# Kernel optimization log

Hardware: AMD Instinct MI355X
Metric: run time of the kernel (lower is better)

## Reference

```python
import jax, jax.numpy as jnp
import numpy as np

HIDDEN = 512
STATE_DIM = 256
H = 8
D = STATE_DIM // H  # 32
B = 8
T = 4096


def setup_inputs() -> dict:
    key = jax.random.key(0)
    ks = jax.random.split(key, 12)
    s = 0.02
    return {
        "hidden_states": jax.random.normal(ks[0], (B, T, HIDDEN), jnp.float32),
        "state": jnp.zeros((B, H, D, D), jnp.float32),
        "W_k": jax.random.normal(ks[1], (STATE_DIM, HIDDEN), jnp.float32) * s,
        "W_v": jax.random.normal(ks[2], (STATE_DIM, HIDDEN), jnp.float32) * s,
        "W_q": jax.random.normal(ks[3], (STATE_DIM, HIDDEN), jnp.float32) * s,
        "W_beta": jax.random.normal(ks[4], (STATE_DIM, HIDDEN), jnp.float32) * s,
        "b_beta": jnp.zeros((STATE_DIM,), jnp.float32),
        "W_alpha": jax.random.normal(ks[5], (STATE_DIM, HIDDEN), jnp.float32) * s,
        "b_alpha": jnp.full((STATE_DIM,), 2.0, jnp.float32),
        "W_out": jax.random.normal(ks[6], (HIDDEN, STATE_DIM), jnp.float32) * s,
        "gate_W": jax.random.normal(ks[7], (STATE_DIM, HIDDEN), jnp.float32) * s,
        "norm_w": jnp.ones((STATE_DIM,), jnp.float32),
    }


def _rms_norm(x, w, eps=1e-6):
    dtype = x.dtype
    xf = x.astype(jnp.float32)
    n = xf * jax.lax.rsqrt(jnp.mean(xf * xf, axis=-1, keepdims=True) + eps)
    return (n * w).astype(dtype)


def reference(hidden_states, state, W_k, W_v, W_q, W_beta, b_beta, W_alpha, b_alpha, W_out, gate_W, norm_w):
    bsz, seq_len, _ = hidden_states.shape
    # projections -> (B, T, H, D)
    k = (hidden_states @ W_k.T).reshape(bsz, seq_len, H, D)
    v = (hidden_states @ W_v.T).reshape(bsz, seq_len, H, D)
    q = (hidden_states @ W_q.T).reshape(bsz, seq_len, H, D)
    beta = jax.nn.sigmoid(hidden_states @ W_beta.T + b_beta).reshape(bsz, seq_len, H, D)
    alpha = jax.nn.sigmoid(hidden_states @ W_alpha.T + b_alpha).reshape(bsz, seq_len, H, D)
    # F.normalize(k, dim=-1) with eps=1e-12
    k = k / jnp.maximum(jnp.linalg.norm(k, axis=-1, keepdims=True), 1e-12)
    gate = hidden_states @ gate_W.T  # (B, T, STATE_DIM)

    # time-major for scan: (T, B, H, D)
    def tm(x):
        return jnp.swapaxes(x, 0, 1)

    def step(S, inp):
        k_t, v_t, q_t, b_t, a_t = inp
        S = S * a_t[..., None]                              # row-wise decay
        pred = jnp.einsum('bhij,bhj->bhi', S, k_t)
        S = S + jnp.einsum('bhi,bhj->bhij', b_t * (v_t - pred), k_t)
        readout = jnp.einsum('bhij,bhj->bhi', S, q_t)       # (B, H, D)
        return S, readout

    S_final, readouts = jax.lax.scan(step, state, (tm(k), tm(v), tm(q), tm(beta), tm(alpha)))
    context = jnp.swapaxes(readouts, 0, 1).reshape(bsz, seq_len, STATE_DIM)
    context = _rms_norm(context, norm_w) * jax.nn.silu(gate)
    output = context @ W_out.T
    return output, S_final
```

## Files before the change

kernel.cpp:

```cpp
#include <hip/hip_runtime.h>
#include <stdint.h>

#define B_    8
#define T_    4096
#define HID   512
#define SD    256
#define NH    8
#define HD    32
#define M_TOK (B_*T_)

typedef __attribute__((ext_vector_type(8))) short short8;
typedef __attribute__((ext_vector_type(4))) float f32x4;
typedef __attribute__((ext_vector_type(4))) float f4;
typedef __attribute__((ext_vector_type(2))) float f2;

__device__ __forceinline__ unsigned short f2bf(float f) {
  uint32_t u = __float_as_uint(f);
  uint32_t r = (u + 0x7fffu + ((u >> 16) & 1u)) >> 16;
  return (unsigned short)r;
}

__device__ __forceinline__ void gload16(const void* g, void* l) {
  __builtin_amdgcn_global_load_lds((const __attribute__((address_space(1))) void*)g,
                                   (__attribute__((address_space(3))) void*)l,
                                   16, 0, 0);
}

__device__ __forceinline__ float qred16(float x) {
  x += __int_as_float(__builtin_amdgcn_mov_dpp(__float_as_int(x), 0xB1,  0xF, 0xF, true));
  x += __int_as_float(__builtin_amdgcn_mov_dpp(__float_as_int(x), 0x4E,  0xF, 0xF, true));
  x += __int_as_float(__builtin_amdgcn_mov_dpp(__float_as_int(x), 0x141, 0xF, 0xF, true));
  x += __int_as_float(__builtin_amdgcn_mov_dpp(__float_as_int(x), 0x128, 0xF, 0xF, true));
  return x;
}

__device__ __forceinline__ float dpp_xor1(float x) {
  return __int_as_float(__builtin_amdgcn_mov_dpp(__float_as_int(x), 0xB1, 0xF, 0xF, true));
}

__global__ void cvt_f32_bf16(const float* __restrict__ in, unsigned short* __restrict__ out, int n4) {
  int i = blockIdx.x * blockDim.x + threadIdx.x;
  int stride = gridDim.x * blockDim.x;
  for (; i < n4; i += stride) {
    float4 v = reinterpret_cast<const float4*>(in)[i];
    ushort4 o;
    o.x = f2bf(v.x); o.y = f2bf(v.y); o.z = f2bf(v.z); o.w = f2bf(v.w);
    reinterpret_cast<ushort4*>(out)[i] = o;
  }
}

__global__ void __launch_bounds__(256) cvt_weights(
    const float* __restrict__ W_k, const float* __restrict__ W_v,
    const float* __restrict__ W_q, const float* __restrict__ W_beta,
    const float* __restrict__ W_alpha, const float* __restrict__ gate_W,
    const float* __restrict__ W_out,
    unsigned short* __restrict__ Wc, unsigned short* __restrict__ Wob)
{
  int slice = blockIdx.y;
  const float* src = (slice == 0) ? W_k : (slice == 1) ? W_v : (slice == 2) ? W_q :
                     (slice == 3) ? W_beta : (slice == 4) ? W_alpha : (slice == 5) ? gate_W : W_out;
  unsigned short* dst = (slice == 6) ? Wob : (Wc + slice * 131072);
  int i = blockIdx.x * 256 + threadIdx.x;
  float4 v = reinterpret_cast<const float4*>(src)[i];
  ushort4 o;
  o.x = f2bf(v.x); o.y = f2bf(v.y); o.z = f2bf(v.z); o.w = f2bf(v.w);
  reinterpret_cast<ushort4*>(dst)[i] = o;
}

#define PM 128
#define PN 64
#define PK 64

__global__ void __launch_bounds__(256) proj_gemm(
    const unsigned short* __restrict__ hb, const unsigned short* __restrict__ Wc,
    const float* __restrict__ b_beta, const float* __restrict__ b_alpha,
    float* __restrict__ KQi, float* __restrict__ AVBf, float* __restrict__ gate)
{
  __shared__ unsigned short Asm[PM*PK];
  __shared__ unsigned short Bsm[3][PN*PK];
  const int t = threadIdx.x;
  const int w = t >> 6, lane = t & 63;
  const int bm0 = blockIdx.x * PM;
  const int role = blockIdx.y;
  const int grp = role >> 2;
  const int bn0 = (role & 3) * 64;
  const int pr0 = grp ? 4 : 0, pr1 = grp ? 1 : 2, pr2 = grp ? 3 : 5;

  f32x4 acc[3][2][4];
  #pragma unroll
  for (int pp = 0; pp < 3; ++pp)
    #pragma unroll
    for (int i = 0; i < 2; ++i)
      #pragma unroll
      for (int j = 0; j < 4; ++j) acc[pp][i][j] = (f32x4){0.f, 0.f, 0.f, 0.f};

  for (int k0 = 0; k0 < HID; k0 += PK) {
    #pragma unroll
    for (int it = 0; it < 4; ++it) {
      int unit = t + it * 256;
      int row = unit >> 3, seg = unit & 7;
      int dseg = seg ^ (row & 7);
      const unsigned short* g = hb + (size_t)(bm0 + row) * HID + k0 + dseg * 8;
      gload16(g, (char*)Asm + (w * 1024 + it * 4096));
    }
    #pragma unroll
    for (int pp = 0; pp < 3; ++pp) {
      const int pr = (pp == 0) ? pr0 : (pp == 1) ? pr1 : pr2;
      #pragma unroll
      for (int it = 0; it < 2; ++it) {
        int unit = t + it * 256;
        int n = unit >> 3, seg = unit & 7;
        int dseg = seg ^ (n & 7);
        const unsigned short* g = Wc + (size_t)(pr * 256 + bn0 + n) * HID + k0 + dseg * 8;
        gload16(g, (char*)Bsm[pp] + (w * 1024 + it * 4096));
      }
    }
    __syncthreads();
    #pragma unroll
    for (int ks = 0; ks < 2; ++ks) {
      short8 af[2];
      int u = ks * 4 + (lane >> 4);
      int slot = u ^ (lane & 7);
      #pragma unroll
      for (int rb = 0; rb < 2; ++rb) {
        int row = w * 32 + rb * 16 + (lane & 15);
        af[rb] = *(const short8*)((const char*)Asm + row * 128 + slot * 16);
      }
      #pragma unroll
      for (int pp = 0; pp < 3; ++pp) {
        short8 bfr[4];
        #pragma unroll
        for (int cb = 0; cb < 4; ++cb) {
          int nn = cb * 16 + (lane & 15);
          bfr[cb] = *(const short8*)((const char*)Bsm[pp] + nn * 128 + slot * 16);
        }
        #pragma unroll
        for (int rb = 0; rb < 2; ++rb)
          #pragma unroll
          for (int cb = 0; cb < 4; ++cb)
            acc[pp][rb][cb] = __builtin_amdgcn_mfma_f32_16x16x32_bf16(af[rb], bfr[cb], acc[pp][rb][cb], 0, 0, 0);
      }
    }
    __syncthreads();
  }

  if (grp == 0) {
    #pragma unroll
    for (int rb = 0; rb < 2; ++rb) {
      #pragma unroll
      for (int r = 0; r < 4; ++r) {
        float s0 = acc[0][rb][0][r] * acc[0][rb][0][r] + acc[0][rb][1][r] * acc[0][rb][1][r];
        float s1 = acc[0][rb][2][r] * acc[0][rb][2][r] + acc[0][rb][3][r] * acc[0][rb][3][r];
        s0 = qred16(s0); s1 = qred16(s1);
        float i0 = 1.0f / fmaxf(sqrtf(s0), 1e-12f);
        float i1 = 1.0f / fmaxf(sqrtf(s1), 1e-12f);
        acc[0][rb][0][r] *= i0; acc[0][rb][1][r] *= i0;
        acc[0][rb][2][r] *= i1; acc[0][rb][3][r] *= i1;
      }
    }
    #pragma unroll
    for (int rb = 0; rb < 2; ++rb) {
      #pragma unroll
      for (int cb = 0; cb < 4; ++cb) {
        int rem = bn0 + cb * 16 + (lane & 15);
        int h = rem >> 5, d = rem & 31;
        #pragma unroll
        for (int r = 0; r < 4; ++r) {
          int m = bm0 + w * 32 + rb * 16 + (lane >> 4) * 4 + r;
          int bb = m >> 12, tt = m & 4095;
          size_t tok = ((size_t)(bb * NH + h) * T_ + tt);
          float kv = acc[0][rb][cb][r], qv = acc[1][rb][cb][r];
          float kn = dpp_xor1(kv), qn = dpp_xor1(qv);
          if ((lane & 1) == 0)
            *(float4*)&KQi[tok * 64 + (d >> 1) * 4] = (float4){kv, kn, qv, qn};
          gate[(size_t)m * SD + rem] = acc[2][rb][cb][r];
        }
      }
    }
  } else {
    #pragma unroll
    for (int rb = 0; rb < 2; ++rb) {
      #pragma unroll
      for (int cb = 0; cb < 4; ++cb) {
        int rem = bn0 + cb * 16 + (lane & 15);
        int h = rem >> 5, d = rem & 31;
        #pragma unroll
        for (int r = 0; r < 4; ++r) {
          int m = bm0 + w * 32 + rb * 16 + (lane >> 4) * 4 + r;
          int bb = m >> 12, tt = m & 4095;
          size_t tok = ((size_t)(bb * NH + h) * T_ + tt);
          float av = 1.0f / (1.0f + expf(-(acc[0][rb][cb][r] + b_alpha[rem])));
          float vv = acc[1][rb][cb][r];
          float bv = 1.0f / (1.0f + expf(-(acc[2][rb][cb][r] + b_beta[rem])));
          *(float4*)&AVBf[(tok * HD + d) * 4] = (float4){av, vv, bv, 0.0f};
        }
      }
    }
  }
}

#define CH 32
#define NCH (T_/CH)

#define DSR(dst, areg, imm) \
  asm volatile("ds_read_b128 %0, %1 offset:%c2" : "=v"(dst) : "v"(areg), "i"(imm))

#define SHUF2(V,A,B) __builtin_shufflevector(V, V, A, B)

#define BAR asm volatile("s_barrier" ::: "memory")

__global__ void __launch_bounds__(128, 1) scan_kernel(
    const float* __restrict__ KQi, const float4* __restrict__ AVB,
    const float* __restrict__ state_in,
    float* __restrict__ ctx, float* __restrict__ Sfin)
{
  __shared__ __align__(16) char Lds[36864];
  const int blk = blockIdx.x;
  const int bh = blk & 63, rg = blk >> 6;
  const int b = bh >> 3, h = bh & 7;
  const int tid = threadIdx.x;
  const int wid = tid >> 6;
  const int lw = tid & 63;

  const float*  KQg = KQi + (size_t)bh * (T_ * 64);
  const float4* Vg  = AVB + (size_t)bh * (T_ * HD) + rg * 4;

  const uint32_t lds0 = (uint32_t)(uintptr_t)(__attribute__((address_space(3))) char*)&Lds[0];

  if (wid == 1) {
    const int il1 = lw >> 4, tq = lw & 15;
    const uint32_t a_pr = lds0 + 20480 + tq * 256 + il1 * 64;
    float* ctxb = ctx + (size_t)b * T_ * SD + h * HD + rg * 4 + il1;

    const int gpp = lw >> 2, gqt = lw & 3;
    f4 gx0, gx1, gx2, gx3, gy0, gy1, gy2, gy3;
    const uint32_t a_gw = lds0 + 16384 + (2 * gpp) * 64 + gqt * 16 + 12;

    auto stageW = [&](int c2, int buf) {
      const float* kqg = KQg + (size_t)c2 * (CH * 64);
      #pragma unroll
      for (int it = 0; it < 8; ++it)
        gload16(kqg + (size_t)(lw + it * 64) * 4, Lds + buf * 8192 + it * 1024);
      const float4* vg = Vg + (size_t)c2 * (CH * HD);
      #pragma unroll
      for (int it = 0; it < 2; ++it) {
        int tc = it * 16 + (lw >> 2), r = lw & 3;
        gload16(vg + (size_t)tc * HD + r, Lds + 16384 + buf * 2048 + it * 1024);
      }
    };

    auto gfetch = [&](int c2) {
      const float* gp = KQg + ((size_t)c2 * CH + 2 * gpp) * 64 + gqt * 16;
      gx0 = *(const f4*)(gp);      gx1 = *(const f4*)(gp + 4);
      gx2 = *(const f4*)(gp + 8);  gx3 = *(const f4*)(gp + 12);
      gy0 = *(const f4*)(gp + 64); gy1 = *(const f4*)(gp + 68);
      gy2 = *(const f4*)(gp + 72); gy3 = *(const f4*)(gp + 76);
    };

    auto gwrite = [&](int buf) {
      f2 g2 = SHUF2(gx0, 0, 1) * SHUF2(gy0, 0, 1);
      g2 = __builtin_elementwise_fma(SHUF2(gx1, 0, 1), SHUF2(gy1, 0, 1), g2);
      g2 = __builtin_elementwise_fma(SHUF2(gx2, 0, 1), SHUF2(gy2, 0, 1), g2);
      g2 = __builtin_elementwise_fma(SHUF2(gx3, 0, 1), SHUF2(gy3, 0, 1), g2);
      float G = g2.x + g2.y;
      G += __int_as_float(__builtin_amdgcn_mov_dpp(__float_as_int(G), 0xB1, 0xF, 0xF, true));
      G += __int_as_float(__builtin_amdgcn_mov_dpp(__float_as_int(G), 0x4E, 0xF, 0xF, true));
      uint32_t aw = a_gw + buf * 2048;
      asm volatile("ds_write_b32 %0, %1" :: "v"(aw), "v"(G));
      asm volatile("s_waitcnt lgkmcnt(0)" ::: "memory");
    };

#define REDUCE(PB, T0) do { \
      f4 r0_, r1_, r2_, r3_; \
      DSR(r0_, a_pr, (PB)*4096 + 0);  DSR(r1_, a_pr, (PB)*4096 + 16); \
      DSR(r2_, a_pr, (PB)*4096 + 32); DSR(r3_, a_pr, (PB)*4096 + 48); \
      asm volatile("s_waitcnt lgkmcnt(0)" : "+v"(r0_), "+v"(r1_), "+v"(r2_), "+v"(r3_)); \
      f4 s_ = (r0_ + r1_) + (r2_ + r3_); \
      float v_ = (s_.x + s_.y) + (s_.z + s_.w); \
      ctxb[(size_t)((T0) + tq) * SD] = v_; \
    } while (0)

    gfetch(0);
    stageW(0, 0);
    asm volatile("s_waitcnt vmcnt(0)" ::: "memory");
    gwrite(0);
    BAR;
    #pragma unroll 1
    for (int cp = 0; cp < NCH / 2; ++cp) {
      if (cp > 0) REDUCE(2, 64 * cp - 32);
      gfetch(2 * cp + 1);
      stageW(2 * cp + 1, 1);
      BAR;
      if (cp > 0) REDUCE(3, 64 * cp - 16);
      asm volatile("s_waitcnt vmcnt(0)" ::: "memory");
      gwrite(1);
      BAR;
      REDUCE(0, 64 * cp);
      if (cp < NCH / 2 - 1) { gfetch(2 * cp + 2); stageW(2 * cp + 2, 0); }
      BAR;
      REDUCE(1, 64 * cp + 16);
      asm volatile("s_waitcnt vmcnt(0)" ::: "memory");
      if (cp < NCH / 2 - 1) gwrite(0);
      BAR;
    }
    BAR;
    REDUCE(2, T_ - 32);
    REDUCE(3, T_ - 16);
#undef REDUCE
    return;
  }

  const int il = lw >> 4;
  const int p  = lw & 15;

  f2 S2;
  {
    const float* sp = state_in + (size_t)bh * 1024 + (rg * 4 + il) * 32 + p * 2;
    S2 = (f2){sp[0], sp[1]};
  }

  const uint32_t a_kq = lds0 + p * 16;
  const uint32_t a_v  = lds0 + 16384 + il * 16;
  const uint32_t a_pw = lds0 + 20480 + lw * 4;

  f4 kqA, vvA, kqB, vvB, kqC, vvC, kqD, vvD;

#define R2(X, Y, BUF, J) do { \
    DSR(kq##X, a_kq, (BUF)*8192 + (2*(J))*256); \
    DSR(vv##X, a_v,  (BUF)*2048 + (2*(J))*64); \
    DSR(kq##Y, a_kq, (BUF)*8192 + (2*(J)+1)*256); \
    DSR(vv##Y, a_v,  (BUF)*2048 + (2*(J)+1)*64); \
  } while (0)

#define WKA2(N, X, Y) \
    asm volatile("s_waitcnt lgkmcnt(" #N ")" \
                 : "+v"(kq##X), "+v"(vv##X), "+v"(kq##Y), "+v"(vv##Y))

#define C2(X, Y, T0, PB) do { \
    f2 k0_ = SHUF2(kq##X, 0, 1), q0_ = SHUF2(kq##X, 2, 3); \
    f2 k1_ = SHUF2(kq##Y, 0, 1), q1_ = SHUF2(kq##Y, 2, 3); \
    f4 VA_ = vv##X, VB_ = vv##Y; \
    f2 dA_ = k0_ * S2, dB_ = k1_ * S2; \
    float W0_ = qred16(dA_.x + dA_.y); \
    float W1_ = qred16(dB_.x + dB_.y); \
    float u0_ = fmaf(-(VA_.z * VA_.x), W0_, VA_.z * VA_.y); \
    float bua_ = VB_.z * VB_.x; \
    float c2_ = bua_ * VA_.w; \
    float c1_ = fmaf(-(bua_ * VA_.x), W1_, VB_.z * VB_.y); \
    float u1_ = fmaf(-c2_, u0_, c1_); \
    f2 St_ = __builtin_elementwise_fma((f2){u0_, u0_}, k0_, (f2){VA_.x, VA_.x} * S2); \
    f2 Su_ = __builtin_elementwise_fma((f2){u1_, u1_}, k1_, (f2){VB_.x, VB_.x} * St_); \
    f2 o0_ = q0_ * St_; \
    f2 o1_ = q1_ * Su_; \
    float p0_ = o0_.x + o0_.y; \
    float p1_ = o1_.x + o1_.y; \
    S2 = Su_; \
    asm volatile("ds_write_b32 %0, %1 offset:%c2" :: "v"(a_pw), "v"(p0_), "i"((PB)*4096 + ((T0)&15)*256)); \
    asm volatile("ds_write_b32 %0, %1 offset:%c2" :: "v"(a_pw), "v"(p1_), "i"((PB)*4096 + (((T0)+1)&15)*256)); \
  } while (0)

#define CHUNK(BUF, PBa, PBb) do { \
    R2(A,B,BUF,0); R2(C,D,BUF,1); \
    WKA2(4,A,B); C2(A,B, 0,PBa); R2(A,B,BUF,2); \
    WKA2(6,C,D); C2(C,D, 2,PBa); R2(C,D,BUF,3); \
    WKA2(6,A,B); C2(A,B, 4,PBa); R2(A,B,BUF,4); \
    WKA2(6,C,D); C2(C,D, 6,PBa); R2(C,D,BUF,5); \
    WKA2(6,A,B); C2(A,B, 8,PBa); R2(A,B,BUF,6); \
    WKA2(6,C,D); C2(C,D,10,PBa); R2(C,D,BUF,7); \
    WKA2(6,A,B); C2(A,B,12,PBa); R2(A,B,BUF,8); \
    WKA2(6,C,D); C2(C,D,14,PBa); R2(C,D,BUF,9); \
    BAR; \
    WKA2(6,A,B); C2(A,B,16,PBb); R2(A,B,BUF,10); \
    WKA2(6,C,D); C2(C,D,18,PBb); R2(C,D,BUF,11); \
    WKA2(6,A,B); C2(A,B,20,PBb); R2(A,B,BUF,12); \
    WKA2(6,C,D); C2(C,D,22,PBb); R2(C,D,BUF,13); \
    WKA2(6,A,B); C2(A,B,24,PBb); R2(A,B,BUF,14); \
    WKA2(6,C,D); C2(C,D,26,PBb); R2(C,D,BUF,15); \
    WKA2(6,A,B); C2(A,B,28,PBb); \
    WKA2(2,C,D); C2(C,D,30,PBb); \
    BAR; \
  } while (0)

  BAR;
  #pragma unroll 1
  for (int cp = 0; cp < NCH / 2; ++cp) {
    CHUNK(0, 0, 1);
    CHUNK(1, 2, 3);
  }
  asm volatile("s_waitcnt lgkmcnt(0)" ::: "memory");
  BAR;

  {
    float* sp = Sfin + (size_t)bh * 1024 + (rg * 4 + il) * 32 + p * 2;
    sp[0] = S2.x; sp[1] = S2.y;
  }
#undef C2
#undef R2
#undef WKA2
#undef CHUNK
}

__global__ void __launch_bounds__(256) rms_silu(
    const float* __restrict__ ctx, const float* __restrict__ gate,
    const float* __restrict__ norm_w, unsigned short* __restrict__ ctx2)
{
  size_t row = (size_t)blockIdx.x * 4 + (threadIdx.x >> 6);
  int lane = threadIdx.x & 63;
  const float4 x = *(const float4*)&ctx[row * SD + lane * 4];
  float s = x.x * x.x + x.y * x.y + x.z * x.z + x.w * x.w;
  #pragma unroll
  for (int m = 32; m >= 1; m >>= 1) s += __shfl_xor(s, m, 64);
  float rs = 1.0f / sqrtf(s * (1.0f / 256.0f) + 1e-6f);
  const float4 g = *(const float4*)&gate[row * SD + lane * 4];
  const float4 w = *(const float4*)&norm_w[lane * 4];
  ushort4 o;
  o.x = f2bf(x.x * rs * w.x * (g.x / (1.0f + expf(-g.x))));
  o.y = f2bf(x.y * rs * w.y * (g.y / (1.0f + expf(-g.y))));
  o.z = f2bf(x.z * rs * w.z * (g.z / (1.0f + expf(-g.z))));
  o.w = f2bf(x.w * rs * w.w * (g.w / (1.0f + expf(-g.w))));
  *(ushort4*)&ctx2[row * SD + lane * 4] = o;
}

__global__ void __launch_bounds__(256) out_gemm(
    const unsigned short* __restrict__ ctx2, const unsigned short* __restrict__ Wob,
    float* __restrict__ out)
{
  __shared__ unsigned short Asm[PM*PK];
  __shared__ unsigned short Bsm[PN*PK];
  const int t = threadIdx.x;
  const int w = t >> 6, lane = t & 63;
  const int bm0 = blockIdx.x * PM;
  const int bn0 = blockIdx.y * PN;

  f32x4 acc[2][4];
  #pragma unroll
  for (int i = 0; i < 2; ++i)
    #pragma unroll
    for (int j = 0; j < 4; ++j) acc[i][j] = (f32x4){0.f, 0.f, 0.f, 0.f};

  for (int k0 = 0; k0 < SD; k0 += PK) {
    #pragma unroll
    for (int it = 0; it < 4; ++it) {
      int unit = t + it * 256;
      int row = unit >> 3, seg = unit & 7;
      int dseg = seg ^ (row & 7);
      const unsigned short* g = ctx2 + (size_t)(bm0 + row) * SD + k0 + dseg * 8;
      gload16(g, (char*)Asm + (w * 1024 + it * 4096));
    }
    #pragma unroll
    for (int it = 0; it < 2; ++it) {
      int unit = t + it * 256;
      int n = unit >> 3, seg = unit & 7;
      int dseg = seg ^ (n & 7);
      const unsigned short* g = Wob + (size_t)(bn0 + n) * SD + k0 + dseg * 8;
      gload16(g, (char*)Bsm + (w * 1024 + it * 4096));
    }
    __syncthreads();
    #pragma unroll
    for (int ks = 0; ks < 2; ++ks) {
      short8 af[2], bfr[4];
      int u = ks * 4 + (lane >> 4);
      int slot = u ^ (lane & 7);
      #pragma unroll
      for (int rb = 0; rb < 2; ++rb) {
        int row = w * 32 + rb * 16 + (lane & 15);
        af[rb] = *(const short8*)((const char*)Asm + row * 128 + slot * 16);
      }
      #pragma unroll
      for (int cb = 0; cb < 4; ++cb) {
        int nn = cb * 16 + (lane & 15);
        bfr[cb] = *(const short8*)((const char*)Bsm + nn * 128 + slot * 16);
      }
      #pragma unroll
      for (int rb = 0; rb < 2; ++rb)
        #pragma unroll
        for (int cb = 0; cb < 4; ++cb)
          acc[rb][cb] = __builtin_amdgcn_mfma_f32_16x16x32_bf16(af[rb], bfr[cb], acc[rb][cb], 0, 0, 0);
    }
    __syncthreads();
  }
  #pragma unroll
  for (int rb = 0; rb < 2; ++rb)
    #pragma unroll
    for (int cb = 0; cb < 4; ++cb) {
      int n = bn0 + cb * 16 + (lane & 15);
      #pragma unroll
      for (int r = 0; r < 4; ++r) {
        int m = bm0 + w * 32 + rb * 16 + (lane >> 4) * 4 + r;
        out[(size_t)m * 512 + n] = acc[rb][cb][r];
      }
    }
}

extern "C" void kernel_launch(void* const* d_in, const int* in_sizes, int n_in,
                              void* d_out, int out_size, void* d_ws, size_t ws_size,
                              hipStream_t stream) {
  (void)in_sizes; (void)n_in; (void)out_size; (void)ws_size;
  const float* hidden  = (const float*)d_in[0];
  const float* state   = (const float*)d_in[1];
  const float* W_k     = (const float*)d_in[2];
  const float* W_v     = (const float*)d_in[3];
  const float* W_q     = (const float*)d_in[4];
  const float* W_beta  = (const float*)d_in[5];
  const float* b_beta  = (const float*)d_in[6];
  const float* W_alpha = (const float*)d_in[7];
  const float* b_alpha = (const float*)d_in[8];
  const float* W_out   = (const float*)d_in[9];
  const float* gate_W  = (const float*)d_in[10];
  const float* norm_w  = (const float*)d_in[11];
  float* out = (float*)d_out;

  char* ws = (char*)d_ws;
  unsigned short* hb  = (unsigned short*)(ws);
  unsigned short* Wc  = (unsigned short*)(ws + 33554432);
  unsigned short* Wob = (unsigned short*)(ws + 35127296);
  float* KQi  = (float*)(ws + 35389440);
  float* AVBf = (float*)(ws + 102498304);
  unsigned short* ctx2 = (unsigned short*)(ws + 236716032);
  float* ctx  = out;
  float* gate = out + 8388608;
  float* Sfin = out + 16777216;

  cvt_f32_bf16<<<2048, 256, 0, stream>>>(hidden, hb, M_TOK * HID / 4);
  cvt_weights<<<dim3(128, 7), 256, 0, stream>>>(W_k, W_v, W_q, W_beta, W_alpha, gate_W, W_out, Wc, Wob);

  proj_gemm<<<dim3(256, 8), 256, 0, stream>>>(hb, Wc, b_beta, b_alpha, KQi, AVBf, gate);
  scan_kernel<<<512, 128, 0, stream>>>(KQi, (const float4*)AVBf, state, ctx, Sfin);
  rms_silu<<<8192, 256, 0, stream>>>(ctx, gate, norm_w, ctx2);
  out_gemm<<<dim3(256, 8), 256, 0, stream>>>(ctx2, Wob, out);
}
```

Baseline: 432.4 us.

## Reduce scan readouts in compute wave via DPP instead of helper-wave LDS reduction

The compute wave now reduces each readout across the 16 lanes with qred16 and keeps the per-timestep result in a register selected by lane, storing to global once every 16 steps. The helper wave's LDS partial-sum reduction and its extra buffers are dropped, LDS shrinks, and the barrier schedule drops to one per chunk. The aim is to remove LDS write/read traffic and the mid-chunk barrier. In exchange, the serial critical path of the compute wave gains two cross-lane reductions per step.

```diff
diff --git a/kernel.cpp b/kernel.cpp
--- a/kernel.cpp
+++ b/kernel.cpp
@@ -214,7 +214,7 @@
     const float* __restrict__ state_in,
     float* __restrict__ ctx, float* __restrict__ Sfin)
 {
-  __shared__ __align__(16) char Lds[36864];
+  __shared__ __align__(16) char Lds[20480];
   const int blk = blockIdx.x;
   const int bh = blk & 63, rg = blk >> 6;
   const int b = bh >> 3, h = bh & 7;
@@ -228,10 +228,6 @@
   const uint32_t lds0 = (uint32_t)(uintptr_t)(__attribute__((address_space(3))) char*)&Lds[0];
 
   if (wid == 1) {
-    const int il1 = lw >> 4, tq = lw & 15;
-    const uint32_t a_pr = lds0 + 20480 + tq * 256 + il1 * 64;
-    float* ctxb = ctx + (size_t)b * T_ * SD + h * HD + rg * 4 + il1;
-
     const int gpp = lw >> 2, gqt = lw & 3;
     f4 gx0, gx1, gx2, gx3, gy0, gy1, gy2, gy3;
     const uint32_t a_gw = lds0 + 16384 + (2 * gpp) * 64 + gqt * 16 + 12;
@@ -270,43 +266,21 @@
       asm volatile("s_waitcnt lgkmcnt(0)" ::: "memory");
     };
 
-#define REDUCE(PB, T0) do { \
-      f4 r0_, r1_, r2_, r3_; \
-      DSR(r0_, a_pr, (PB)*4096 + 0);  DSR(r1_, a_pr, (PB)*4096 + 16); \
-      DSR(r2_, a_pr, (PB)*4096 + 32); DSR(r3_, a_pr, (PB)*4096 + 48); \
-      asm volatile("s_waitcnt lgkmcnt(0)" : "+v"(r0_), "+v"(r1_), "+v"(r2_), "+v"(r3_)); \
-      f4 s_ = (r0_ + r1_) + (r2_ + r3_); \
-      float v_ = (s_.x + s_.y) + (s_.z + s_.w); \
-      ctxb[(size_t)((T0) + tq) * SD] = v_; \
-    } while (0)
-
     gfetch(0);
     stageW(0, 0);
     asm volatile("s_waitcnt vmcnt(0)" ::: "memory");
     gwrite(0);
     BAR;
     #pragma unroll 1
-    for (int cp = 0; cp < NCH / 2; ++cp) {
-      if (cp > 0) REDUCE(2, 64 * cp - 32);
-      gfetch(2 * cp + 1);
-      stageW(2 * cp + 1, 1);
+    for (int c = 0; c < NCH; ++c) {
+      if (c + 1 < NCH) {
+        gfetch(c + 1);
+        stageW(c + 1, (c + 1) & 1);
+        asm volatile("s_waitcnt vmcnt(0)" ::: "memory");
+        gwrite((c + 1) & 1);
+      }
       BAR;
-      if (cp > 0) REDUCE(3, 64 * cp - 16);
-      asm volatile("s_waitcnt vmcnt(0)" ::: "memory");
-      gwrite(1);
-      BAR;
-      REDUCE(0, 64 * cp);
-      if (cp < NCH / 2 - 1) { gfetch(2 * cp + 2); stageW(2 * cp + 2, 0); }
-      BAR;
-      REDUCE(1, 64 * cp + 16);
-      asm volatile("s_waitcnt vmcnt(0)" ::: "memory");
-      if (cp < NCH / 2 - 1) gwrite(0);
-      BAR;
-    }
-    BAR;
-    REDUCE(2, T_ - 32);
-    REDUCE(3, T_ - 16);
-#undef REDUCE
+    }
     return;
   }
 
@@ -321,7 +295,9 @@
 
   const uint32_t a_kq = lds0 + p * 16;
   const uint32_t a_v  = lds0 + 16384 + il * 16;
-  const uint32_t a_pw = lds0 + 20480 + lw * 4;
+
+  float osel = 0.0f;
+  float* ctxp = ctx + (size_t)b * T_ * SD + (size_t)p * SD + h * HD + rg * 4 + il;
 
   f4 kqA, vvA, kqB, vvB, kqC, vvC, kqD, vvD;
 
@@ -336,7 +312,7 @@
     asm volatile("s_waitcnt lgkmcnt(" #N ")" \
                  : "+v"(kq##X), "+v"(vv##X), "+v"(kq##Y), "+v"(vv##Y))
 
-#define C2(X, Y, T0, PB) do { \
+#define C2(X, Y, T0) do { \
     f2 k0_ = SHUF2(kq##X, 0, 1), q0_ = SHUF2(kq##X, 2, 3); \
     f2 k1_ = SHUF2(kq##Y, 0, 1), q1_ = SHUF2(kq##Y, 2, 3); \
     f4 VA_ = vv##X, VB_ = vv##Y; \
@@ -352,43 +328,41 @@
     f2 Su_ = __builtin_elementwise_fma((f2){u1_, u1_}, k1_, (f2){VB_.x, VB_.x} * St_); \
     f2 o0_ = q0_ * St_; \
     f2 o1_ = q1_ * Su_; \
-    float p0_ = o0_.x + o0_.y; \
-    float p1_ = o1_.x + o1_.y; \
     S2 = Su_; \
-    asm volatile("ds_write_b32 %0, %1 offset:%c2" :: "v"(a_pw), "v"(p0_), "i"((PB)*4096 + ((T0)&15)*256)); \
-    asm volatile("ds_write_b32 %0, %1 offset:%c2" :: "v"(a_pw), "v"(p1_), "i"((PB)*4096 + (((T0)+1)&15)*256)); \
+    float od0_ = qred16(o0_.x + o0_.y); \
+    float od1_ = qred16(o1_.x + o1_.y); \
+    osel = (p == ((T0) & 15))       ? od0_ : osel; \
+    osel = (p == (((T0) + 1) & 15)) ? od1_ : osel; \
+    if ((((T0) + 1) & 15) == 15) { *ctxp = osel; ctxp += 16 * SD; } \
   } while (0)
 
-#define CHUNK(BUF, PBa, PBb) do { \
+#define CHUNK(BUF) do { \
     R2(A,B,BUF,0); R2(C,D,BUF,1); \
-    WKA2(4,A,B); C2(A,B, 0,PBa); R2(A,B,BUF,2); \
-    WKA2(6,C,D); C2(C,D, 2,PBa); R2(C,D,BUF,3); \
-    WKA2(6,A,B); C2(A,B, 4,PBa); R2(A,B,BUF,4); \
-    WKA2(6,C,D); C2(C,D, 6,PBa); R2(C,D,BUF,5); \
-    WKA2(6,A,B); C2(A,B, 8,PBa); R2(A,B,BUF,6); \
-    WKA2(6,C,D); C2(C,D,10,PBa); R2(C,D,BUF,7); \
-    WKA2(6,A,B); C2(A,B,12,PBa); R2(A,B,BUF,8); \
-    WKA2(6,C,D); C2(C,D,14,PBa); R2(C,D,BUF,9); \
-    BAR; \
-    WKA2(6,A,B); C2(A,B,16,PBb); R2(A,B,BUF,10); \
-    WKA2(6,C,D); C2(C,D,18,PBb); R2(C,D,BUF,11); \
-    WKA2(6,A,B); C2(A,B,20,PBb); R2(A,B,BUF,12); \
-    WKA2(6,C,D); C2(C,D,22,PBb); R2(C,D,BUF,13); \
-    WKA2(6,A,B); C2(A,B,24,PBb); R2(A,B,BUF,14); \
-    WKA2(6,C,D); C2(C,D,26,PBb); R2(C,D,BUF,15); \
-    WKA2(6,A,B); C2(A,B,28,PBb); \
-    WKA2(2,C,D); C2(C,D,30,PBb); \
+    WKA2(4,A,B); C2(A,B, 0); R2(A,B,BUF,2); \
+    WKA2(4,C,D); C2(C,D, 2); R2(C,D,BUF,3); \
+    WKA2(4,A,B); C2(A,B, 4); R2(A,B,BUF,4); \
+    WKA2(4,C,D); C2(C,D, 6); R2(C,D,BUF,5); \
+    WKA2(4,A,B); C2(A,B, 8); R2(A,B,BUF,6); \
+    WKA2(4,C,D); C2(C,D,10); R2(C,D,BUF,7); \
+    WKA2(4,A,B); C2(A,B,12); R2(A,B,BUF,8); \
+    WKA2(4,C,D); C2(C,D,14); R2(C,D,BUF,9); \
+    WKA2(4,A,B); C2(A,B,16); R2(A,B,BUF,10); \
+    WKA2(4,C,D); C2(C,D,18); R2(C,D,BUF,11); \
+    WKA2(4,A,B); C2(A,B,20); R2(A,B,BUF,12); \
+    WKA2(4,C,D); C2(C,D,22); R2(C,D,BUF,13); \
+    WKA2(4,A,B); C2(A,B,24); R2(A,B,BUF,14); \
+    WKA2(4,C,D); C2(C,D,26); R2(C,D,BUF,15); \
+    WKA2(4,A,B); C2(A,B,28); \
+    WKA2(0,C,D); C2(C,D,30); \
     BAR; \
   } while (0)
 
   BAR;
   #pragma unroll 1
   for (int cp = 0; cp < NCH / 2; ++cp) {
-    CHUNK(0, 0, 1);
-    CHUNK(1, 2, 3);
-  }
-  asm volatile("s_waitcnt lgkmcnt(0)" ::: "memory");
-  BAR;
+    CHUNK(0);
+    CHUNK(1);
+  }
 
   {
     float* sp = Sfin + (size_t)bh * 1024 + (rg * 4 + il) * 32 + p * 2;
```

Result: faster. 401.5 us (-7.1%).
